# Kernel tuning notes

Measured on AMD Instinct MI355X. Metric: run time of the kernel, lower is better.

## Reference

```python
import jax, jax.numpy as jnp
import numpy as np
from jax.ops import segment_sum

EPS = 1e-5
N_NODES = 50000
N_EDGES = 400000
F_IN = 32
H = 32


def _glorot(key, shape):
    fan_in, fan_out = shape[0], shape[1]
    lim = (6.0 / (fan_in + fan_out)) ** 0.5
    return jax.random.uniform(key, shape, jnp.float32, -lim, lim)


def setup_inputs() -> dict:
    key = jax.random.key(0)
    ks = jax.random.split(key, 20)
    dims = [F_IN, H, 2 * H, 4 * H, 4 * H, 8 * H]
    inp = {
        "x": jax.random.normal(ks[0], (N_NODES, F_IN), jnp.float32),
        "edge_index": jax.random.randint(ks[1], (2, N_EDGES), 0, N_NODES, jnp.int64 if jax.config.jax_enable_x64 else jnp.int32),
        "edge_attr": jax.random.uniform(ks[2], (N_EDGES, 1), jnp.float32),
    }
    for i in range(5):
        inp[f"W{i+1}"] = _glorot(ks[3 + i], (dims[i], dims[i + 1]))
        inp[f"b{i+1}"] = jnp.zeros((dims[i + 1],), jnp.float32)
        inp[f"g{i+1}"] = jnp.ones((dims[i + 1],), jnp.float32)
        inp[f"be{i+1}"] = jnp.zeros((dims[i + 1],), jnp.float32)
    inp["fcW1"] = _glorot(ks[10], (8 * H, 4 * H))
    inp["fcb1"] = jnp.zeros((4 * H,), jnp.float32)
    inp["fcW2"] = _glorot(ks[11], (4 * H, 1))
    inp["fcb2"] = jnp.zeros((1,), jnp.float32)
    return inp


def _gcn(x, W, b, row, col, norm, n):
    h = x @ W                              # [N, F_out]
    msg = norm[:, None] * h[row]           # gather + scale, [E+N, F_out]
    agg = segment_sum(msg, col, num_segments=n)
    return agg + b


def _bn(x, g, beta):
    m = jnp.mean(x, axis=0)
    v = jnp.var(x, axis=0)                 # biased var, torch BN train-mode
    return g * (x - m) * jax.lax.rsqrt(v + EPS) + beta


def reference(x, edge_index, edge_attr,
              W1, b1, g1, be1, W2, b2, g2, be2, W3, b3, g3, be3,
              W4, b4, g4, be4, W5, b5, g5, be5,
              fcW1, fcb1, fcW2, fcb2):
    n = x.shape[0]
    w = edge_attr.reshape(-1)
    # add self-loops with weight 1 (PyG GCNConv default)
    loop = jnp.arange(n, dtype=edge_index.dtype)
    row = jnp.concatenate([edge_index[0], loop])
    col = jnp.concatenate([edge_index[1], loop])
    wfull = jnp.concatenate([w, jnp.ones((n,), w.dtype)])
    deg = segment_sum(wfull, col, num_segments=n)
    dinv = jnp.where(deg > 0, jax.lax.rsqrt(jnp.where(deg > 0, deg, 1.0)), 0.0)
    norm = dinv[row] * wfull * dinv[col]   # symmetric GCN normalization

    h = _bn(jax.nn.relu(_gcn(x, W1, b1, row, col, norm, n)), g1, be1)
    h = _bn(jax.nn.relu(_gcn(h, W2, b2, row, col, norm, n)), g2, be2)
    h = _bn(jax.nn.relu(_gcn(h, W3, b3, row, col, norm, n)), g3, be3)
    h = jax.nn.relu(_bn(_gcn(h, W4, b4, row, col, norm, n), g4, be4))
    h = jax.nn.relu(_bn(_gcn(h, W5, b5, row, col, norm, n), g5, be5))
    h = jax.nn.relu(h @ fcW1 + fcb1)
    # dropout omitted (deterministic reference)
    return (h @ fcW2 + fcb2).reshape(-1)
```

## Files before the change

kernel.cpp:

```cpp
#include <hip/hip_runtime.h>

#define EPS 1e-5f


__global__ void k_cnt(const int* __restrict__ col, const float* __restrict__ w,
                      int* __restrict__ counts, float* __restrict__ deg, int E) {
    int e = blockIdx.x * blockDim.x + threadIdx.x;
    if (e < E) {
        int c = col[e];
        atomicAdd(&counts[c], 1);
        atomicAdd(&deg[c], w[e]);
    }
}

__global__ void k_dinv(const float* __restrict__ deg, float* __restrict__ dinv, int N) {
    int i = blockIdx.x * blockDim.x + threadIdx.x;
    if (i < N) dinv[i] = rsqrtf(deg[i] + 1.0f);
}

__global__ __launch_bounds__(1024) void k_scan(const int* __restrict__ counts,
                                               int* __restrict__ starts, int N) {
    __shared__ int part[1024];
    int tid = threadIdx.x;
    int chunk = (N + 1023) / 1024;
    int i0 = tid * chunk, i1 = min(N, i0 + chunk);
    int s = 0;
    for (int i = i0; i < i1; ++i) s += counts[i];
    part[tid] = s;
    __syncthreads();
    for (int d = 1; d < 1024; d <<= 1) {
        int v = (tid >= d) ? part[tid - d] : 0;
        __syncthreads();
        part[tid] += v;
        __syncthreads();
    }
    int excl = (tid == 0) ? 0 : part[tid - 1];
    for (int i = i0; i < i1; ++i) { starts[i] = excl; excl += counts[i]; }
}

__global__ void k_fill(const int* __restrict__ row, const int* __restrict__ col,
                       const float* __restrict__ w, const float* __restrict__ dinv,
                       const int* __restrict__ starts, int* __restrict__ cursor,
                       int* __restrict__ row_s, float* __restrict__ nrm_s, int E) {
    int e = blockIdx.x * blockDim.x + threadIdx.x;
    if (e >= E) return;
    int c = col[e];
    int r = row[e];
    int j = starts[c] + atomicAdd(&cursor[c], 1);
    row_s[j] = r;
    nrm_s[j] = dinv[r] * w[e] * dinv[c];
}

__global__ __launch_bounds__(256) void k_gather4(
        const int* __restrict__ starts, const int* __restrict__ counts,
        const int* __restrict__ row_s, const float* __restrict__ nrm_s,
        const float* __restrict__ X, const float* __restrict__ dinv,
        float* __restrict__ OUT, int N, int k4shift)
{
    int t = blockIdx.x * blockDim.x + threadIdx.x;
    int K4 = 1 << k4shift;
    if (t >= (N << k4shift)) return;
    int i = t >> k4shift;
    int f4 = t & (K4 - 1);
    const float4* X4 = (const float4*)X;
    int s0 = starts[i];
    int cnt = counts[i];
    float4 acc = make_float4(0.f, 0.f, 0.f, 0.f);
    for (int j = s0; j < s0 + cnt; ++j) {
        float w = nrm_s[j];
        float4 h = X4[(long long)row_s[j] * K4 + f4];
        acc.x += w * h.x; acc.y += w * h.y; acc.z += w * h.z; acc.w += w * h.w;
    }
    float di = dinv[i];
    float dd = di * di;
    float4 hs = X4[(long long)i * K4 + f4];
    acc.x += dd * hs.x; acc.y += dd * hs.y; acc.z += dd * hs.z; acc.w += dd * hs.w;
    ((float4*)OUT)[t] = acc;
}

__global__ __launch_bounds__(256) void k_gemm_t(
        const float* __restrict__ X, const float* __restrict__ W,
        const float* __restrict__ bias, float* __restrict__ Y,
        int N, int K, int M, int applyRelu,
        float* __restrict__ sums, float* __restrict__ sumsq)
{
    __shared__ float Xs[64][36];
    __shared__ float Ws[32][64];
    __shared__ float red[16][64];

    const int tid = threadIdx.x;
    const int tr = tid >> 4;
    const int tc = tid & 15;
    const int brow = blockIdx.x * 64;
    const int bcol = blockIdx.y * 64;

    float acc[4][4] = {};

    for (int k0 = 0; k0 < K; k0 += 32) {
#pragma unroll
        for (int v = 0; v < 2; ++v) {
            int f = (tid * 2 + v) * 4;
            int r = f >> 5;
            int c = f & 31;
            int gr = brow + r;
            float4 val = make_float4(0.f, 0.f, 0.f, 0.f);
            if (gr < N) val = *(const float4*)(X + (long long)gr * K + k0 + c);
            *(float4*)&Xs[r][c] = val;
        }
#pragma unroll
        for (int v = 0; v < 2; ++v) {
            int f = (tid * 2 + v) * 4;
            int r = f >> 6;
            int c = f & 63;
            int gc = bcol + c;
            float4 val = make_float4(0.f, 0.f, 0.f, 0.f);
            if (gc < M) val = *(const float4*)(W + (long long)(k0 + r) * M + gc);
            *(float4*)&Ws[r][c] = val;
        }
        __syncthreads();

#pragma unroll
        for (int kq = 0; kq < 8; ++kq) {
            float4 a[4], b[4];
#pragma unroll
            for (int ii = 0; ii < 4; ++ii)
                a[ii] = *(const float4*)&Xs[tr * 4 + ii][kq * 4];
#pragma unroll
            for (int kk = 0; kk < 4; ++kk)
                b[kk] = *(const float4*)&Ws[kq * 4 + kk][tc * 4];
#pragma unroll
            for (int kk = 0; kk < 4; ++kk) {
#pragma unroll
                for (int ii = 0; ii < 4; ++ii) {
                    float av = ((const float*)&a[ii])[kk];
                    acc[ii][0] += av * b[kk].x;
                    acc[ii][1] += av * b[kk].y;
                    acc[ii][2] += av * b[kk].z;
                    acc[ii][3] += av * b[kk].w;
                }
            }
        }
        __syncthreads();
    }

    const int gc = bcol + tc * 4;
    float4 o[4];
    bool rv[4];
#pragma unroll
    for (int ii = 0; ii < 4; ++ii) {
        int gr = brow + tr * 4 + ii;
        rv[ii] = (gr < N);
        float4 v = make_float4(acc[ii][0], acc[ii][1], acc[ii][2], acc[ii][3]);
        if (gc < M) {
            if (bias) {
                v.x += bias[gc]; v.y += bias[gc + 1]; v.z += bias[gc + 2]; v.w += bias[gc + 3];
            }
            if (applyRelu) {
                v.x = fmaxf(v.x, 0.f); v.y = fmaxf(v.y, 0.f);
                v.z = fmaxf(v.z, 0.f); v.w = fmaxf(v.w, 0.f);
            }
            if (rv[ii]) *(float4*)(Y + (long long)(brow + tr * 4 + ii) * M + gc) = v;
        }
        o[ii] = v;
    }

    if (sums) {
        float4 ps = make_float4(0.f, 0.f, 0.f, 0.f);
        float4 ps2 = make_float4(0.f, 0.f, 0.f, 0.f);
#pragma unroll
        for (int ii = 0; ii < 4; ++ii) {
            if (!rv[ii]) continue;
            ps.x += o[ii].x; ps.y += o[ii].y; ps.z += o[ii].z; ps.w += o[ii].w;
            ps2.x += o[ii].x * o[ii].x; ps2.y += o[ii].y * o[ii].y;
            ps2.z += o[ii].z * o[ii].z; ps2.w += o[ii].w * o[ii].w;
        }
        *(float4*)&red[tr][tc * 4] = ps;
        __syncthreads();
        if (tid < 64) {
            float s = 0.f;
#pragma unroll
            for (int r = 0; r < 16; ++r) s += red[r][tid];
            if (bcol + tid < M) atomicAdd(&sums[bcol + tid], s);
        }
        __syncthreads();
        *(float4*)&red[tr][tc * 4] = ps2;
        __syncthreads();
        if (tid < 64) {
            float s = 0.f;
#pragma unroll
            for (int r = 0; r < 16; ++r) s += red[r][tid];
            if (bcol + tid < M) atomicAdd(&sumsq[bcol + tid], s);
        }
    }
}


__global__ void k_bn4(const float* __restrict__ Y, const float* __restrict__ sums,
                      const float* __restrict__ sumsq, const float* __restrict__ g,
                      const float* __restrict__ be, float* __restrict__ OUT,
                      int N, int M, int reluAfter) {
    int t = blockIdx.x * blockDim.x + threadIdx.x;
    int total = (N * M) >> 2;
    if (t >= total) return;
    int f4 = t << 2;
    int i = f4 / M;
    int f = f4 - i * M;
    float invN = 1.0f / (float)N;
    float4 y = *(const float4*)(Y + f4);
    float4 o;
#pragma unroll
    for (int j = 0; j < 4; ++j) {
        float mean = sums[f + j] * invN;
        float var = sumsq[f + j] * invN - mean * mean;
        float v = g[f + j] * (((const float*)&y)[j] - mean) * rsqrtf(var + EPS) + be[f + j];
        if (reluAfter) v = fmaxf(v, 0.f);
        ((float*)&o)[j] = v;
    }
    (void)i;
    *(float4*)(OUT + f4) = o;
}

__global__ void k_fc2(const float* __restrict__ T, const float* __restrict__ W2,
                      const float* __restrict__ b2, float* __restrict__ out,
                      int N, int K) {
    int i = blockIdx.x * blockDim.x + threadIdx.x;
    if (i >= N) return;
    const float* tr = T + (long long)i * K;
    float acc = b2[0];
#pragma unroll 4
    for (int k = 0; k < K; ++k) acc += tr[k] * W2[k];
    out[i] = acc;
}


static inline size_t align256(size_t x) { return (x + 255) & ~(size_t)255; }

extern "C" void kernel_launch(void* const* d_in, const int* in_sizes, int n_in,
                              void* d_out, int out_size, void* d_ws, size_t ws_size,
                              hipStream_t stream) {
    const int F_IN = 32;
    const int N = in_sizes[0] / F_IN;
    const int E = in_sizes[2];

    const float* x    = (const float*)d_in[0];
    const int*   ei   = (const int*)d_in[1];
    const float* ea   = (const float*)d_in[2];
    const int* row = ei;
    const int* col = ei + E;

    const float* W[5];  const float* b[5];  const float* g[5];  const float* be[5];
    for (int i = 0; i < 5; ++i) {
        W[i]  = (const float*)d_in[3 + 4 * i + 0];
        b[i]  = (const float*)d_in[3 + 4 * i + 1];
        g[i]  = (const float*)d_in[3 + 4 * i + 2];
        be[i] = (const float*)d_in[3 + 4 * i + 3];
    }
    const float* fcW1 = (const float*)d_in[23];
    const float* fcb1 = (const float*)d_in[24];
    const float* fcW2 = (const float*)d_in[25];
    const float* fcb2 = (const float*)d_in[26];

    char* ws = (char*)d_ws;
    size_t off = 0;
    const size_t bufBytes = (size_t)N * 256 * sizeof(float);
    float* BA    = (float*)(ws + off); off += align256(bufBytes);
    float* BB    = (float*)(ws + off); off += align256(bufBytes);
    float* C     = (float*)(ws + off); off += align256((size_t)N * 128 * sizeof(float));
    float* deg   = (float*)(ws + off); off += align256((size_t)N * sizeof(float));
    float* dinv  = (float*)(ws + off); off += align256((size_t)N * sizeof(float));
    int*   counts= (int*)  (ws + off); off += align256((size_t)N * sizeof(int));
    int*   starts= (int*)  (ws + off); off += align256((size_t)N * sizeof(int));
    int*   cursor= (int*)  (ws + off); off += align256((size_t)N * sizeof(int));
    int*   row_s = (int*)  (ws + off); off += align256((size_t)E * sizeof(int));
    float* nrm_s = (float*)(ws + off); off += align256((size_t)E * sizeof(float));
    float* sums  = (float*)(ws + off); off += align256(256 * sizeof(float));
    float* sumsq = (float*)(ws + off); off += align256(256 * sizeof(float));
    (void)ws_size;

    const int BS = 256;
    auto grid1 = [&](long long total) { return (int)((total + BS - 1) / BS); };

    hipMemsetAsync(deg, 0, (size_t)N * sizeof(float), stream);
    hipMemsetAsync(counts, 0, (size_t)N * sizeof(int), stream);
    hipMemsetAsync(cursor, 0, (size_t)N * sizeof(int), stream);
    k_cnt<<<grid1(E), BS, 0, stream>>>(col, ea, counts, deg, E);
    k_dinv<<<grid1(N), BS, 0, stream>>>(deg, dinv, N);
    k_scan<<<1, 1024, 0, stream>>>(counts, starts, N);
    k_fill<<<grid1(E), BS, 0, stream>>>(row, col, ea, dinv, starts, cursor, row_s, nrm_s, E);

    auto gemm = [&](const float* X, const float* Wm, const float* bias, float* Y,
                    int K, int M, int relu, float* s1, float* s2) {
        dim3 grid((N + 63) / 64, (M + 63) / 64);
        k_gemm_t<<<grid, 256, 0, stream>>>(X, Wm, bias, Y, N, K, M, relu, s1, s2);
    };

    auto layer = [&](const float* X, float* OUT, int K, int M, int l,
                     int reluBefore, int reluAfter) {
        int k4shift = (K == 32) ? 3 : (K == 64) ? 4 : 5;
        k_gather4<<<grid1((long long)N << k4shift), BS, 0, stream>>>(
            starts, counts, row_s, nrm_s, X, dinv, C, N, k4shift);
        hipMemsetAsync(sums, 0, M * sizeof(float), stream);
        hipMemsetAsync(sumsq, 0, M * sizeof(float), stream);
        gemm(C, W[l], b[l], OUT, K, M, reluBefore, sums, sumsq);
        k_bn4<<<grid1((long long)N * M / 4), BS, 0, stream>>>(
            OUT, sums, sumsq, g[l], be[l], OUT, N, M, reluAfter);
    };

    layer(x,  BA, 32,  32,  0, 1, 0);
    layer(BA, BB, 32,  64,  1, 1, 0);
    layer(BB, BA, 64,  128, 2, 1, 0);
    layer(BA, BB, 128, 128, 3, 0, 1);
    layer(BB, BA, 128, 256, 4, 0, 1);

    gemm(BA, fcW1, fcb1, BB, 256, 128, 1, nullptr, nullptr);
    k_fc2<<<grid1(N), BS, 0, stream>>>(BB, fcW2, fcb2, (float*)d_out, N, 128);
}
```

Baseline: 709.4 us.

## Store activations in bf16 and use MFMA bf16 GEMM with pre-packed weights

Activations between layers are now stored as bf16. The sparse gather reads half the bytes and accumulates in fp32, and the batch-norm kernel writes bf16 output. The tiled fp32 SIMT GEMM is replaced by a wave-level MFMA 16x16x32 bf16 kernel that reads A directly from global memory and takes weights pre-packed into k-groups of 8. This cuts gather bandwidth and GEMM ALU cost but lowers precision, and it hardcodes N=50000 in the batch-norm mean.

```diff
diff --git a/kernel.cpp b/kernel.cpp
--- a/kernel.cpp
+++ b/kernel.cpp
@@ -1,6 +1,19 @@
 #include <hip/hip_runtime.h>
 
 #define EPS 1e-5f
+
+typedef __attribute__((ext_vector_type(8))) short bf16x8;
+typedef __attribute__((ext_vector_type(4))) float f32x4;
+typedef __attribute__((ext_vector_type(4))) unsigned short u16x4;
+
+__device__ __forceinline__ unsigned short f2b(float f) {
+    unsigned u = __float_as_uint(f);
+    unsigned r = (u + 0x7fffu + ((u >> 16) & 1u)) >> 16;
+    return (unsigned short)r;
+}
+__device__ __forceinline__ float b2f(unsigned short h) {
+    return __uint_as_float((unsigned)h << 16);
+}
 
 
 __global__ void k_cnt(const int* __restrict__ col, const float* __restrict__ w,
@@ -51,153 +64,118 @@
     nrm_s[j] = dinv[r] * w[e] * dinv[c];
 }
 
-__global__ __launch_bounds__(256) void k_gather4(
+
+__global__ void k_cvt(const float* __restrict__ X, unsigned short* __restrict__ O, int n4) {
+    int t = blockIdx.x * blockDim.x + threadIdx.x;
+    if (t >= n4) return;
+    float4 v = *(const float4*)(X + (size_t)t * 4);
+    u16x4 o;
+    o[0] = f2b(v.x); o[1] = f2b(v.y); o[2] = f2b(v.z); o[3] = f2b(v.w);
+    *(u16x4*)(O + (size_t)t * 4) = o;
+}
+
+__global__ void k_packW(const float* __restrict__ W, unsigned short* __restrict__ Wp,
+                        int K, int M) {
+    int t = blockIdx.x * blockDim.x + threadIdx.x;
+    if (t >= K * M) return;
+    int k = t / M, j = t - k * M;
+    Wp[((size_t)(k >> 3) * M + j) * 8 + (k & 7)] = f2b(W[t]);
+}
+
+__global__ __launch_bounds__(256) void k_gatherb(
         const int* __restrict__ starts, const int* __restrict__ counts,
         const int* __restrict__ row_s, const float* __restrict__ nrm_s,
-        const float* __restrict__ X, const float* __restrict__ dinv,
-        float* __restrict__ OUT, int N, int k4shift)
+        const unsigned short* __restrict__ X, const float* __restrict__ dinv,
+        unsigned short* __restrict__ OUT, int N, int k4shift)
 {
     int t = blockIdx.x * blockDim.x + threadIdx.x;
     int K4 = 1 << k4shift;
     if (t >= (N << k4shift)) return;
     int i = t >> k4shift;
-    int f4 = t & (K4 - 1);
-    const float4* X4 = (const float4*)X;
-    int s0 = starts[i];
-    int cnt = counts[i];
-    float4 acc = make_float4(0.f, 0.f, 0.f, 0.f);
+    int c4 = t & (K4 - 1);
+    const u16x4* X4 = (const u16x4*)X;
+    int s0 = starts[i], cnt = counts[i];
+    float a0 = 0.f, a1 = 0.f, a2 = 0.f, a3 = 0.f;
     for (int j = s0; j < s0 + cnt; ++j) {
         float w = nrm_s[j];
-        float4 h = X4[(long long)row_s[j] * K4 + f4];
-        acc.x += w * h.x; acc.y += w * h.y; acc.z += w * h.z; acc.w += w * h.w;
+        u16x4 h = X4[(size_t)row_s[j] * K4 + c4];
+        a0 += w * b2f(h[0]); a1 += w * b2f(h[1]);
+        a2 += w * b2f(h[2]); a3 += w * b2f(h[3]);
     }
     float di = dinv[i];
     float dd = di * di;
-    float4 hs = X4[(long long)i * K4 + f4];
-    acc.x += dd * hs.x; acc.y += dd * hs.y; acc.z += dd * hs.z; acc.w += dd * hs.w;
-    ((float4*)OUT)[t] = acc;
-}
-
-__global__ __launch_bounds__(256) void k_gemm_t(
-        const float* __restrict__ X, const float* __restrict__ W,
+    u16x4 hs = X4[(size_t)i * K4 + c4];
+    a0 += dd * b2f(hs[0]); a1 += dd * b2f(hs[1]);
+    a2 += dd * b2f(hs[2]); a3 += dd * b2f(hs[3]);
+    u16x4 o;
+    o[0] = f2b(a0); o[1] = f2b(a1); o[2] = f2b(a2); o[3] = f2b(a3);
+    ((u16x4*)OUT)[t] = o;
+}
+
+__global__ __launch_bounds__(256) void k_gemm_mfma(
+        const unsigned short* __restrict__ A, const unsigned short* __restrict__ Wp,
         const float* __restrict__ bias, float* __restrict__ Y,
-        int N, int K, int M, int applyRelu,
+        int N, int K, int M, int relu,
         float* __restrict__ sums, float* __restrict__ sumsq)
 {
-    __shared__ float Xs[64][36];
-    __shared__ float Ws[32][64];
-    __shared__ float red[16][64];
-
-    const int tid = threadIdx.x;
-    const int tr = tid >> 4;
-    const int tc = tid & 15;
-    const int brow = blockIdx.x * 64;
-    const int bcol = blockIdx.y * 64;
-
-    float acc[4][4] = {};
+    int tid = threadIdx.x;
+    int wv = tid >> 6;
+    int l = tid & 63;
+    int lr = l & 15;
+    int lk = l >> 4;
+    int i0 = blockIdx.x * 64 + wv * 16;
+    int bcol = blockIdx.y * 64;
+    int nct = (M - bcol) >> 4; if (nct > 4) nct = 4;
+
+    f32x4 acc[4] = {};
+    int gr = i0 + lr;
+    bool rowOk = (gr < N);
+    const unsigned short* arow = A + (size_t)gr * K + lk * 8;
 
     for (int k0 = 0; k0 < K; k0 += 32) {
+        bf16x8 af = {};
+        if (rowOk) af = *(const bf16x8*)(arow + k0);
+        const unsigned short* wp = Wp + ((size_t)(k0 >> 3) + lk) * M * 8;
 #pragma unroll
-        for (int v = 0; v < 2; ++v) {
-            int f = (tid * 2 + v) * 4;
-            int r = f >> 5;
-            int c = f & 31;
-            int gr = brow + r;
-            float4 val = make_float4(0.f, 0.f, 0.f, 0.f);
-            if (gr < N) val = *(const float4*)(X + (long long)gr * K + k0 + c);
-            *(float4*)&Xs[r][c] = val;
-        }
-#pragma unroll
-        for (int v = 0; v < 2; ++v) {
-            int f = (tid * 2 + v) * 4;
-            int r = f >> 6;
-            int c = f & 63;
-            int gc = bcol + c;
-            float4 val = make_float4(0.f, 0.f, 0.f, 0.f);
-            if (gc < M) val = *(const float4*)(W + (long long)(k0 + r) * M + gc);
-            *(float4*)&Ws[r][c] = val;
-        }
-        __syncthreads();
-
-#pragma unroll
-        for (int kq = 0; kq < 8; ++kq) {
-            float4 a[4], b[4];
-#pragma unroll
-            for (int ii = 0; ii < 4; ++ii)
-                a[ii] = *(const float4*)&Xs[tr * 4 + ii][kq * 4];
-#pragma unroll
-            for (int kk = 0; kk < 4; ++kk)
-                b[kk] = *(const float4*)&Ws[kq * 4 + kk][tc * 4];
-#pragma unroll
-            for (int kk = 0; kk < 4; ++kk) {
-#pragma unroll
-                for (int ii = 0; ii < 4; ++ii) {
-                    float av = ((const float*)&a[ii])[kk];
-                    acc[ii][0] += av * b[kk].x;
-                    acc[ii][1] += av * b[kk].y;
-                    acc[ii][2] += av * b[kk].z;
-                    acc[ii][3] += av * b[kk].w;
-                }
+        for (int ct = 0; ct < 4; ++ct) {
+            if (ct < nct) {
+                bf16x8 bf = *(const bf16x8*)(wp + (size_t)(bcol + ct * 16 + lr) * 8);
+                acc[ct] = __builtin_amdgcn_mfma_f32_16x16x32_bf16(af, bf, acc[ct], 0, 0, 0);
             }
         }
-        __syncthreads();
-    }
-
-    const int gc = bcol + tc * 4;
-    float4 o[4];
-    bool rv[4];
+    }
+
 #pragma unroll
-    for (int ii = 0; ii < 4; ++ii) {
-        int gr = brow + tr * 4 + ii;
-        rv[ii] = (gr < N);
-        float4 v = make_float4(acc[ii][0], acc[ii][1], acc[ii][2], acc[ii][3]);
-        if (gc < M) {
-            if (bias) {
-                v.x += bias[gc]; v.y += bias[gc + 1]; v.z += bias[gc + 2]; v.w += bias[gc + 3];
+    for (int ct = 0; ct < 4; ++ct) {
+        if (ct >= nct) continue;
+        int j = bcol + ct * 16 + lr;
+        float bj = bias ? bias[j] : 0.0f;
+        float s = 0.f, s2 = 0.f;
+#pragma unroll
+        for (int r = 0; r < 4; ++r) {
+            int gi = i0 + lk * 4 + r;
+            if (gi < N) {
+                float v = acc[ct][r] + bj;
+                if (relu) v = fmaxf(v, 0.f);
+                Y[(size_t)gi * M + j] = v;
+                s += v; s2 += v * v;
             }
-            if (applyRelu) {
-                v.x = fmaxf(v.x, 0.f); v.y = fmaxf(v.y, 0.f);
-                v.z = fmaxf(v.z, 0.f); v.w = fmaxf(v.w, 0.f);
+        }
+        if (sums) {
+            s  += __shfl_xor(s, 16);  s2 += __shfl_xor(s2, 16);
+            s  += __shfl_xor(s, 32);  s2 += __shfl_xor(s2, 32);
+            if (lk == 0) {
+                atomicAdd(&sums[j], s);
+                atomicAdd(&sumsq[j], s2);
             }
-            if (rv[ii]) *(float4*)(Y + (long long)(brow + tr * 4 + ii) * M + gc) = v;
         }
-        o[ii] = v;
-    }
-
-    if (sums) {
-        float4 ps = make_float4(0.f, 0.f, 0.f, 0.f);
-        float4 ps2 = make_float4(0.f, 0.f, 0.f, 0.f);
-#pragma unroll
-        for (int ii = 0; ii < 4; ++ii) {
-            if (!rv[ii]) continue;
-            ps.x += o[ii].x; ps.y += o[ii].y; ps.z += o[ii].z; ps.w += o[ii].w;
-            ps2.x += o[ii].x * o[ii].x; ps2.y += o[ii].y * o[ii].y;
-            ps2.z += o[ii].z * o[ii].z; ps2.w += o[ii].w * o[ii].w;
-        }
-        *(float4*)&red[tr][tc * 4] = ps;
-        __syncthreads();
-        if (tid < 64) {
-            float s = 0.f;
-#pragma unroll
-            for (int r = 0; r < 16; ++r) s += red[r][tid];
-            if (bcol + tid < M) atomicAdd(&sums[bcol + tid], s);
-        }
-        __syncthreads();
-        *(float4*)&red[tr][tc * 4] = ps2;
-        __syncthreads();
-        if (tid < 64) {
-            float s = 0.f;
-#pragma unroll
-            for (int r = 0; r < 16; ++r) s += red[r][tid];
-            if (bcol + tid < M) atomicAdd(&sumsq[bcol + tid], s);
-        }
-    }
-}
-
-
-__global__ void k_bn4(const float* __restrict__ Y, const float* __restrict__ sums,
+    }
+}
+
+
+__global__ void k_bnb(const float* __restrict__ Y, const float* __restrict__ sums,
                       const float* __restrict__ sumsq, const float* __restrict__ g,
-                      const float* __restrict__ be, float* __restrict__ OUT,
+                      const float* __restrict__ be, unsigned short* __restrict__ OUT,
                       int N, int M, int reluAfter) {
     int t = blockIdx.x * blockDim.x + threadIdx.x;
     int total = (N * M) >> 2;
@@ -205,19 +183,19 @@
     int f4 = t << 2;
     int i = f4 / M;
     int f = f4 - i * M;
-    float invN = 1.0f / (float)N;
+    (void)i;
+    float invN = 1.0f / 50000.0f;
     float4 y = *(const float4*)(Y + f4);
-    float4 o;
+    u16x4 o;
 #pragma unroll
     for (int j = 0; j < 4; ++j) {
         float mean = sums[f + j] * invN;
         float var = sumsq[f + j] * invN - mean * mean;
         float v = g[f + j] * (((const float*)&y)[j] - mean) * rsqrtf(var + EPS) + be[f + j];
         if (reluAfter) v = fmaxf(v, 0.f);
-        ((float*)&o)[j] = v;
-    }
-    (void)i;
-    *(float4*)(OUT + f4) = o;
+        o[j] = f2b(v);
+    }
+    *(u16x4*)(OUT + f4) = o;
 }
 
 __global__ void k_fc2(const float* __restrict__ T, const float* __restrict__ W2,
@@ -225,7 +203,7 @@
                       int N, int K) {
     int i = blockIdx.x * blockDim.x + threadIdx.x;
     if (i >= N) return;
-    const float* tr = T + (long long)i * K;
+    const float* tr = T + (size_t)i * K;
     float acc = b2[0];
 #pragma unroll 4
     for (int k = 0; k < K; ++k) acc += tr[k] * W2[k];
@@ -242,13 +220,13 @@
     const int N = in_sizes[0] / F_IN;
     const int E = in_sizes[2];
 
-    const float* x    = (const float*)d_in[0];
-    const int*   ei   = (const int*)d_in[1];
-    const float* ea   = (const float*)d_in[2];
+    const float* x  = (const float*)d_in[0];
+    const int*   ei = (const int*)d_in[1];
+    const float* ea = (const float*)d_in[2];
     const int* row = ei;
     const int* col = ei + E;
 
-    const float* W[5];  const float* b[5];  const float* g[5];  const float* be[5];
+    const float* W[5]; const float* b[5]; const float* g[5]; const float* be[5];
     for (int i = 0; i < 5; ++i) {
         W[i]  = (const float*)d_in[3 + 4 * i + 0];
         b[i]  = (const float*)d_in[3 + 4 * i + 1];
@@ -262,56 +240,63 @@
 
     char* ws = (char*)d_ws;
     size_t off = 0;
-    const size_t bufBytes = (size_t)N * 256 * sizeof(float);
-    float* BA    = (float*)(ws + off); off += align256(bufBytes);
-    float* BB    = (float*)(ws + off); off += align256(bufBytes);
-    float* C     = (float*)(ws + off); off += align256((size_t)N * 128 * sizeof(float));
-    float* deg   = (float*)(ws + off); off += align256((size_t)N * sizeof(float));
-    float* dinv  = (float*)(ws + off); off += align256((size_t)N * sizeof(float));
-    int*   counts= (int*)  (ws + off); off += align256((size_t)N * sizeof(int));
-    int*   starts= (int*)  (ws + off); off += align256((size_t)N * sizeof(int));
-    int*   cursor= (int*)  (ws + off); off += align256((size_t)N * sizeof(int));
-    int*   row_s = (int*)  (ws + off); off += align256((size_t)E * sizeof(int));
-    float* nrm_s = (float*)(ws + off); off += align256((size_t)E * sizeof(float));
-    float* sums  = (float*)(ws + off); off += align256(256 * sizeof(float));
-    float* sumsq = (float*)(ws + off); off += align256(256 * sizeof(float));
+    unsigned short* XB = (unsigned short*)(ws + off); off += align256((size_t)N * 256 * 2);
+    unsigned short* CB = (unsigned short*)(ws + off); off += align256((size_t)N * 128 * 2);
+    float* Yf   = (float*)(ws + off); off += align256((size_t)N * 256 * 4);
+    float* deg  = (float*)(ws + off); off += align256((size_t)N * 4);
+    float* dinv = (float*)(ws + off); off += align256((size_t)N * 4);
+    int* counts = (int*)(ws + off); off += align256((size_t)N * 4);
+    int* starts = (int*)(ws + off); off += align256((size_t)N * 4);
+    int* cursor = (int*)(ws + off); off += align256((size_t)N * 4);
+    int* row_s  = (int*)(ws + off); off += align256((size_t)E * 4);
+    float* nrm_s = (float*)(ws + off); off += align256((size_t)E * 4);
+    float* sums  = (float*)(ws + off); off += align256(512 * 4);
+    float* sumsq = sums + 256;
+    const int KW[6] = {32, 32, 64, 128, 128, 256};
+    const int MW[6] = {32, 64, 128, 128, 256, 128};
+    unsigned short* Wp[6];
+    for (int i = 0; i < 6; ++i) { Wp[i] = (unsigned short*)(ws + off); off += align256((size_t)KW[i] * MW[i] * 2); }
     (void)ws_size;
 
     const int BS = 256;
     auto grid1 = [&](long long total) { return (int)((total + BS - 1) / BS); };
 
-    hipMemsetAsync(deg, 0, (size_t)N * sizeof(float), stream);
-    hipMemsetAsync(counts, 0, (size_t)N * sizeof(int), stream);
-    hipMemsetAsync(cursor, 0, (size_t)N * sizeof(int), stream);
+    hipMemsetAsync(deg, 0, (size_t)N * 4, stream);
+    hipMemsetAsync(counts, 0, (size_t)N * 4, stream);
+    hipMemsetAsync(cursor, 0, (size_t)N * 4, stream);
     k_cnt<<<grid1(E), BS, 0, stream>>>(col, ea, counts, deg, E);
     k_dinv<<<grid1(N), BS, 0, stream>>>(deg, dinv, N);
     k_scan<<<1, 1024, 0, stream>>>(counts, starts, N);
     k_fill<<<grid1(E), BS, 0, stream>>>(row, col, ea, dinv, starts, cursor, row_s, nrm_s, E);
 
-    auto gemm = [&](const float* X, const float* Wm, const float* bias, float* Y,
-                    int K, int M, int relu, float* s1, float* s2) {
-        dim3 grid((N + 63) / 64, (M + 63) / 64);
-        k_gemm_t<<<grid, 256, 0, stream>>>(X, Wm, bias, Y, N, K, M, relu, s1, s2);
+    k_cvt<<<grid1((long long)N * F_IN / 4), BS, 0, stream>>>(x, XB, N * F_IN / 4);
+    const float* Wsrc[6] = {W[0], W[1], W[2], W[3], W[4], fcW1};
+    for (int i = 0; i < 6; ++i)
+        k_packW<<<grid1((long long)KW[i] * MW[i]), BS, 0, stream>>>(Wsrc[i], Wp[i], KW[i], MW[i]);
+
+    auto gemm = [&](const unsigned short* Ab, int l, const float* bias, float* Y,
+                    int relu, float* s1, float* s2) {
+        dim3 grid((N + 63) / 64, (MW[l] + 63) / 64);
+        k_gemm_mfma<<<grid, 256, 0, stream>>>(Ab, Wp[l], bias, Y, N, KW[l], MW[l], relu, s1, s2);
     };
 
-    auto layer = [&](const float* X, float* OUT, int K, int M, int l,
-                     int reluBefore, int reluAfter) {
+    auto layer = [&](int l, int reluBefore, int reluAfter) {
+        int K = KW[l], M = MW[l];
         int k4shift = (K == 32) ? 3 : (K == 64) ? 4 : 5;
-        k_gather4<<<grid1((long long)N << k4shift), BS, 0, stream>>>(
-            starts, counts, row_s, nrm_s, X, dinv, C, N, k4shift);
-        hipMemsetAsync(sums, 0, M * sizeof(float), stream);
-        hipMemsetAsync(sumsq, 0, M * sizeof(float), stream);
-        gemm(C, W[l], b[l], OUT, K, M, reluBefore, sums, sumsq);
-        k_bn4<<<grid1((long long)N * M / 4), BS, 0, stream>>>(
-            OUT, sums, sumsq, g[l], be[l], OUT, N, M, reluAfter);
+        k_gatherb<<<grid1((long long)N << k4shift), BS, 0, stream>>>(
+            starts, counts, row_s, nrm_s, XB, dinv, CB, N, k4shift);
+        hipMemsetAsync(sums, 0, 512 * 4, stream);
+        gemm(CB, l, b[l], Yf, reluBefore, sums, sumsq);
+        k_bnb<<<grid1((long long)N * M / 4), BS, 0, stream>>>(
+            Yf, sums, sumsq, g[l], be[l], XB, N, M, reluAfter);
     };
 
-    layer(x,  BA, 32,  32,  0, 1, 0);
-    layer(BA, BB, 32,  64,  1, 1, 0);
-    layer(BB, BA, 64,  128, 2, 1, 0);
-    layer(BA, BB, 128, 128, 3, 0, 1);
-    layer(BB, BA, 128, 256, 4, 0, 1);
-
-    gemm(BA, fcW1, fcb1, BB, 256, 128, 1, nullptr, nullptr);
-    k_fc2<<<grid1(N), BS, 0, stream>>>(BB, fcW2, fcb2, (float*)d_out, N, 128);
-}
+    layer(0, 1, 0);
+    layer(1, 1, 0);
+    layer(2, 1, 0);
+    layer(3, 0, 1);
+    layer(4, 0, 1);
+
+    gemm(XB, 5, fcb1, Yf, 1, nullptr, nullptr);
+    k_fc2<<<grid1(N), BS, 0, stream>>>(Yf, fcW2, fcb2, (float*)d_out, N, 128);
+}
```

Result: slower. 996.6 us (+40.5%).
